# Kernel optimization log

Measured on AMD Instinct MI355X. Metric: run time of the kernel, lower is better.

Reference implementation:

```python
import jax, jax.numpy as jnp
import numpy as np


def setup_inputs() -> dict:
    key = jax.random.key(0)
    k1, k2, k3, k4, k5 = jax.random.split(key, 5)
    C, Cr = 512, 64  # in_channels, in_channels // 8
    B, W, H = 16, 64, 64
    x = jax.random.normal(k1, (B, C, W, H), dtype=jnp.float32)
    # 1x1 conv == pointwise linear over channels; store as [out, in]
    w1 = jax.random.normal(k2, (Cr, C), dtype=jnp.float32) * (1.0 / np.sqrt(C))
    b1 = jax.random.normal(k3, (Cr,), dtype=jnp.float32) * 0.01
    w2 = jax.random.normal(k4, (C, Cr), dtype=jnp.float32) * (1.0 / np.sqrt(Cr))
    b2 = jax.random.normal(k5, (C,), dtype=jnp.float32) * 0.01
    return {"x": x, "w1": w1, "b1": b1, "w2": w2, "b2": b2}


def reference(x, w1, b1, w2, b2):
    B, C, W, H = x.shape
    # conv1x1: channel reduction C -> C//8
    r = jnp.einsum('bchw,oc->bohw', x, w1) + b1[None, :, None, None]
    q = r.reshape(B, -1, W * H)                      # [B, C', N] query/key/value
    # channel-channel attention map [B, C', C'] (bmm(query, key^T))
    att = jnp.einsum('bcn,bdn->bcd', q, q)
    att = jax.nn.softmax(att, axis=-1)
    out = jnp.einsum('bcd,bdn->bcn', att, q)          # [B, C', N]
    out = out.reshape(B, -1, W, H)
    # conv_out: channel expansion C//8 -> C, plus residual
    out = jnp.einsum('bchw,oc->bohw', out, w2) + b2[None, :, None, None]
    return out + x
```

## Files before the change

### kernel.cpp

```cpp
#include <hip/hip_runtime.h>
#include <math.h>

#define NPIX 4096
#define CIN  512
#define CR   64
#define NB   16

typedef __bf16 bf16x8 __attribute__((ext_vector_type(8)));
typedef float  f32x4  __attribute__((ext_vector_type(4)));
typedef float  f32x16 __attribute__((ext_vector_type(16)));
typedef unsigned int uint;
typedef uint   uint4v __attribute__((ext_vector_type(4)));
typedef unsigned short ushort;

static const size_t W1B_OFF = 0;
static const size_t Q_OFF   = W1B_OFF + 65536;
static const size_t QT_OFF  = Q_OFF  + (size_t)NB*CR*NPIX*2;
static const size_t ATT_OFF = QT_OFF + (size_t)NB*NPIX*CR*2;
static const size_t MB_OFF  = ATT_OFF + (size_t)NB*CR*CR*4;


static __device__ inline uint pk_bf16(float a, float b) {
    uint r;
    asm volatile("v_cvt_pk_bf16_f32 %0, %1, %2" : "=v"(r) : "v"(a), "v"(b));
    return r;
}

__global__ __launch_bounds__(256) void k0_cast(const float* __restrict__ w1,
                                               uint* __restrict__ w1b) {
    int i = blockIdx.x * 256 + threadIdx.x;
    w1b[i] = pk_bf16(w1[2 * i], w1[2 * i + 1]);
}

#define K1_LOAD(XV, AF, KS) do {                                             \
    int k0_ = (KS) * 32 + kg * 8;                                            \
    _Pragma("unroll")                                                        \
    for (int pf = 0; pf < 4; pf++) {                                         \
        const float* xp_ = xb + (size_t)k0_ * NPIX + pf * 16;                \
        _Pragma("unroll")                                                    \
        for (int j = 0; j < 8; j++) XV[pf][j] = xp_[(size_t)j * NPIX];       \
    }                                                                        \
    _Pragma("unroll")                                                        \
    for (int of = 0; of < 4; of++)                                           \
        AF[of] = *(const bf16x8*)(w1b + (size_t)(of * 16 + lo) * CIN + k0_); \
} while (0)

#define K1_COMPUTE(XV, AF) do {                                              \
    _Pragma("unroll")                                                        \
    for (int pf = 0; pf < 4; pf++) {                                         \
        uint4v bu_;                                                          \
        _Pragma("unroll")                                                    \
        for (int j = 0; j < 4; j++)                                          \
            bu_[j] = pk_bf16(XV[pf][2 * j], XV[pf][2 * j + 1]);              \
        bf16x8 bf_ = __builtin_bit_cast(bf16x8, bu_);                        \
        _Pragma("unroll")                                                    \
        for (int of = 0; of < 4; of++)                                       \
            acc[pf][of] = __builtin_amdgcn_mfma_f32_16x16x32_bf16(           \
                AF[of], bf_, acc[pf][of], 0, 0, 0);                          \
    }                                                                        \
} while (0)

__global__ __launch_bounds__(256) void k1_conv1(const float* __restrict__ x,
                                                const ushort* __restrict__ w1b,
                                                const float* __restrict__ b1,
                                                ushort* __restrict__ q,
                                                uint2* __restrict__ qt4) {
    int b = blockIdx.y;
    int t = threadIdx.x;
    int wid = t >> 6, l = t & 63;
    int lo = l & 15, kg = l >> 4;
    int px0 = blockIdx.x * 256 + wid * 64;
    const float* xb = x + (size_t)b * CIN * NPIX + px0 + lo;

    f32x4 acc[4][4] = {};
    float xvA[4][8], xvB[4][8];
    bf16x8 afA[4], afB[4];

    K1_LOAD(xvA, afA, 0);
#pragma unroll
    for (int ks2 = 0; ks2 < 8; ks2++) {
        K1_LOAD(xvB, afB, 2 * ks2 + 1);
        K1_COMPUTE(xvA, afA);
        if (ks2 < 7) K1_LOAD(xvA, afA, 2 * ks2 + 2);
        K1_COMPUTE(xvB, afB);
    }

#pragma unroll
    for (int pf = 0; pf < 4; pf++) {
        int px = px0 + pf * 16 + lo;
        ushort* qb = q + (size_t)b * CR * NPIX + px;
        uint2* qt4b = qt4 + (((size_t)b * 256 + (px0 >> 4) + pf) * 4) * 64 + kg * 16 + lo;
#pragma unroll
        for (int of = 0; of < 4; of++) {
            int o = of * 16 + kg * 4;
            float v0 = acc[pf][of][0] + b1[o + 0];
            float v1 = acc[pf][of][1] + b1[o + 1];
            float v2 = acc[pf][of][2] + b1[o + 2];
            float v3 = acc[pf][of][3] + b1[o + 3];
            uint p0 = pk_bf16(v0, v1), p1 = pk_bf16(v2, v3);
            qb[(size_t)(o + 0) * NPIX] = (ushort)(p0 & 0xffff);
            qb[(size_t)(o + 1) * NPIX] = (ushort)(p0 >> 16);
            qb[(size_t)(o + 2) * NPIX] = (ushort)(p1 & 0xffff);
            qb[(size_t)(o + 3) * NPIX] = (ushort)(p1 >> 16);
            qt4b[of * 64] = make_uint2(p0, p1);
        }
    }
}

__global__ __launch_bounds__(1024) void k2_att(const ushort* __restrict__ q,
                                               float* __restrict__ att) {
    __shared__ float part[8][64][66];
    int b = blockIdx.x;
    int t = threadIdx.x;
    int w = t >> 6, l = t & 63;
    int lo = l & 15, kg = l >> 4;
    const ushort* qb = q + (size_t)b * CR * NPIX + w * 256;

    f32x4 acc[4][4] = {};
#pragma unroll 2
    for (int ks = 0; ks < 8; ks++) {
        bf16x8 fr[4];
#pragma unroll
        for (int cf = 0; cf < 4; cf++)
            fr[cf] = *(const bf16x8*)(qb + (size_t)(cf * 16 + lo) * NPIX + ks * 32 + kg * 8);
#pragma unroll
        for (int cf = 0; cf < 4; cf++)
#pragma unroll
            for (int df = 0; df < 4; df++)
                acc[cf][df] = __builtin_amdgcn_mfma_f32_16x16x32_bf16(fr[cf], fr[df], acc[cf][df], 0, 0, 0);
    }
    if (w < 8) {
#pragma unroll
        for (int cf = 0; cf < 4; cf++)
#pragma unroll
            for (int df = 0; df < 4; df++)
#pragma unroll
                for (int r = 0; r < 4; r++)
                    part[w][cf * 16 + kg * 4 + r][df * 16 + lo] = acc[cf][df][r];
    }
    __syncthreads();
    if (w >= 8) {
        int ws = w - 8;
#pragma unroll
        for (int cf = 0; cf < 4; cf++)
#pragma unroll
            for (int df = 0; df < 4; df++)
#pragma unroll
                for (int r = 0; r < 4; r++)
                    part[ws][cf * 16 + kg * 4 + r][df * 16 + lo] += acc[cf][df][r];
    }
    __syncthreads();

#pragma unroll
    for (int i = 0; i < 4; i++) {
        int c = w * 4 + i;
        float v = 0.f;
#pragma unroll
        for (int pw = 0; pw < 8; pw++) v += part[pw][c][l];
        float m = v;
#pragma unroll
        for (int s = 1; s < 64; s <<= 1) m = fmaxf(m, __shfl_xor(m, s, 64));
        float e = __expf(v - m);
        float ssum = e;
#pragma unroll
        for (int s = 1; s < 64; s <<= 1) ssum += __shfl_xor(ssum, s, 64);
        att[((size_t)b * CR + c) * CR + l] = e / ssum;
    }
}

__global__ __launch_bounds__(256) void k3_m(const float* __restrict__ w2,
                                            const float* __restrict__ att,
                                            ushort* __restrict__ mb) {
    int b = blockIdx.y;
    int c  = (blockIdx.x >> 2) * 256 + threadIdx.x;
    int dg = (blockIdx.x & 3) * 16;
    const float* ab  = att + (size_t)b * CR * CR + dg;
    const float* w2r = w2 + (size_t)c * CR;
    float acc[16];
#pragma unroll
    for (int j = 0; j < 16; j++) acc[j] = 0.f;
    for (int k = 0; k < CR; k++) {
        float wv = w2r[k];
#pragma unroll
        for (int j4 = 0; j4 < 4; j4++) {
            f32x4 av = *(const f32x4*)(ab + k * CR + j4 * 4);
#pragma unroll
            for (int u = 0; u < 4; u++)
                acc[j4 * 4 + u] = fmaf(wv, av[u], acc[j4 * 4 + u]);
        }
    }
    uint* mp = (uint*)(mb + ((size_t)b * CIN + c) * CR + dg);
#pragma unroll
    for (int i = 0; i < 8; i++)
        mp[i] = pk_bf16(acc[2 * i], acc[2 * i + 1]);
}

#define K4_LOAD(AF, XR, CC8) do {                                            \
    int c0_ = (cch * 8 + (CC8)) * 32;                                        \
    const ushort* mrow_ = mb + ((size_t)b * CIN + c0_ + l31) * CR;           \
    _Pragma("unroll")                                                        \
    for (int ks = 0; ks < 4; ks++)                                           \
        AF[ks] = *(const bf16x8*)(mrow_ + ks * 16 + lhi * 8);                \
    _Pragma("unroll")                                                        \
    for (int r = 0; r < 16; r++) {                                           \
        int rowD_ = (r & 3) + 8 * (r >> 2) + 4 * lhi;                        \
        XR[r] = x[((size_t)b * CIN + c0_ + rowD_) * NPIX + px];              \
    }                                                                        \
} while (0)

#define K4_STORE(AF, XR, CC8) do {                                           \
    int c0_ = (cch * 8 + (CC8)) * 32;                                        \
    f32x16 acc_ = {};                                                        \
    _Pragma("unroll")                                                        \
    for (int ks = 0; ks < 4; ks++)                                           \
        acc_ = __builtin_amdgcn_mfma_f32_32x32x16_bf16(AF[ks], bf[ks], acc_, 0, 0, 0); \
    _Pragma("unroll")                                                        \
    for (int r = 0; r < 16; r++) {                                           \
        int rowD_ = (r & 3) + 8 * (r >> 2) + 4 * lhi;                        \
        int c_ = c0_ + rowD_;                                                \
        size_t off_ = ((size_t)b * CIN + c_) * NPIX + px;                    \
        y[off_] = acc_[r] + b2[c_] + XR[r];                                  \
    }                                                                        \
} while (0)

__global__ __launch_bounds__(256) void k4_out(const uint2* __restrict__ qt4,
                                              const ushort* __restrict__ mb,
                                              const float* __restrict__ b2,
                                              const float* __restrict__ x,
                                              float* __restrict__ y) {
    int cch = blockIdx.x;
    int b = blockIdx.z;
    int t = threadIdx.x;
    int wid = t >> 6, l = t & 63;
    int l31 = l & 31, lhi = l >> 5;
    int pxblk = blockIdx.y * 128 + wid * 32;
    int px = pxblk + l31;
    const uint2* qt4b = qt4 + (size_t)b * 65536;
    int pxhi = (pxblk >> 4) + ((l >> 4) & 1);
    int pxlo = l & 15;
    int kg2 = lhi * 2;

    bf16x8 bf[4];
#pragma unroll
    for (int ks = 0; ks < 4; ks++) {
        const uint2* p_ = qt4b + (((size_t)pxhi * 4 + ks) * 4 + kg2) * 16 + pxlo;
        uint2 g0 = p_[0], g1 = p_[16];
        uint4v u; u[0] = g0.x; u[1] = g0.y; u[2] = g1.x; u[3] = g1.y;
        bf[ks] = __builtin_bit_cast(bf16x8, u);
    }

    bf16x8 afA[4], afB[4];
    float xrA[16], xrB[16];
    K4_LOAD(afA, xrA, 0);
#pragma unroll
    for (int i2 = 0; i2 < 4; i2++) {
        K4_LOAD(afB, xrB, 2 * i2 + 1);
        K4_STORE(afA, xrA, 2 * i2);
        if (i2 < 3) K4_LOAD(afA, xrA, 2 * i2 + 2);
        K4_STORE(afB, xrB, 2 * i2 + 1);
    }
}

extern "C" void kernel_launch(void* const* d_in, const int* in_sizes, int n_in,
                              void* d_out, int out_size, void* d_ws, size_t ws_size,
                              hipStream_t stream) {
    const float* x  = (const float*)d_in[0];
    const float* w1 = (const float*)d_in[1];
    const float* b1 = (const float*)d_in[2];
    const float* w2 = (const float*)d_in[3];
    const float* b2 = (const float*)d_in[4];
    float* y = (float*)d_out;
    char* ws = (char*)d_ws;

    uint*   w1b = (uint*)  (ws + W1B_OFF);
    ushort* q   = (ushort*)(ws + Q_OFF);
    uint2*  qt4 = (uint2*) (ws + QT_OFF);
    float*  att = (float*) (ws + ATT_OFF);
    ushort* mb  = (ushort*)(ws + MB_OFF);

    hipLaunchKernelGGL(k0_cast,  dim3(64),         dim3(256),  0, stream, w1, w1b);
    hipLaunchKernelGGL(k1_conv1, dim3(16, 16),     dim3(256),  0, stream, x, (const ushort*)w1b, b1, q, qt4);
    hipLaunchKernelGGL(k2_att,   dim3(16),         dim3(1024), 0, stream, q, att);
    hipLaunchKernelGGL(k3_m,     dim3(8, 16),      dim3(256),  0, stream, w2, att, mb);
    hipLaunchKernelGGL(k4_out,   dim3(2, 32, 16),  dim3(256),  0, stream, qt4, mb, b2, x, y);
}
```

Measured before the change: 113.8 us.

## Fuse w1 bf16 cast into conv1 and give each k4 block all output channels

Drops the separate w1 cast kernel: conv1 now loads fp32 w1 directly and converts it to bf16 in registers before each MFMA. The output kernel no longer splits the channel dimension across two blocks, so each block loops over all 16 channel chunks and reads its q tile only once. This removes one launch and halves the k4 grid, but adds redundant weight conversion in every conv1 block and lowers parallelism in k4.

```diff
diff --git a/kernel.cpp b/kernel.cpp
--- a/kernel.cpp
+++ b/kernel.cpp
@@ -13,8 +13,7 @@
 typedef uint   uint4v __attribute__((ext_vector_type(4)));
 typedef unsigned short ushort;
 
-static const size_t W1B_OFF = 0;
-static const size_t Q_OFF   = W1B_OFF + 65536;
+static const size_t Q_OFF   = 65536;
 static const size_t QT_OFF  = Q_OFF  + (size_t)NB*CR*NPIX*2;
 static const size_t ATT_OFF = QT_OFF + (size_t)NB*NPIX*CR*2;
 static const size_t MB_OFF  = ATT_OFF + (size_t)NB*CR*CR*4;
@@ -26,13 +25,7 @@
     return r;
 }
 
-__global__ __launch_bounds__(256) void k0_cast(const float* __restrict__ w1,
-                                               uint* __restrict__ w1b) {
-    int i = blockIdx.x * 256 + threadIdx.x;
-    w1b[i] = pk_bf16(w1[2 * i], w1[2 * i + 1]);
-}
-
-#define K1_LOAD(XV, AF, KS) do {                                             \
+#define K1_LOAD(XV, WF, KS) do {                                             \
     int k0_ = (KS) * 32 + kg * 8;                                            \
     _Pragma("unroll")                                                        \
     for (int pf = 0; pf < 4; pf++) {                                         \
@@ -41,11 +34,24 @@
         for (int j = 0; j < 8; j++) XV[pf][j] = xp_[(size_t)j * NPIX];       \
     }                                                                        \
     _Pragma("unroll")                                                        \
-    for (int of = 0; of < 4; of++)                                           \
-        AF[of] = *(const bf16x8*)(w1b + (size_t)(of * 16 + lo) * CIN + k0_); \
-} while (0)
-
-#define K1_COMPUTE(XV, AF) do {                                              \
+    for (int of = 0; of < 4; of++) {                                         \
+        const float* wp_ = w1 + (size_t)(of * 16 + lo) * CIN + k0_;          \
+        WF[of][0] = *(const f32x4*)wp_;                                      \
+        WF[of][1] = *(const f32x4*)(wp_ + 4);                                \
+    }                                                                        \
+} while (0)
+
+#define K1_COMPUTE(XV, WF) do {                                              \
+    bf16x8 af_[4];                                                           \
+    _Pragma("unroll")                                                        \
+    for (int of = 0; of < 4; of++) {                                         \
+        uint4v au_;                                                          \
+        au_[0] = pk_bf16(WF[of][0][0], WF[of][0][1]);                        \
+        au_[1] = pk_bf16(WF[of][0][2], WF[of][0][3]);                        \
+        au_[2] = pk_bf16(WF[of][1][0], WF[of][1][1]);                        \
+        au_[3] = pk_bf16(WF[of][1][2], WF[of][1][3]);                        \
+        af_[of] = __builtin_bit_cast(bf16x8, au_);                           \
+    }                                                                        \
     _Pragma("unroll")                                                        \
     for (int pf = 0; pf < 4; pf++) {                                         \
         uint4v bu_;                                                          \
@@ -56,12 +62,12 @@
         _Pragma("unroll")                                                    \
         for (int of = 0; of < 4; of++)                                       \
             acc[pf][of] = __builtin_amdgcn_mfma_f32_16x16x32_bf16(           \
-                AF[of], bf_, acc[pf][of], 0, 0, 0);                          \
+                af_[of], bf_, acc[pf][of], 0, 0, 0);                         \
     }                                                                        \
 } while (0)
 
 __global__ __launch_bounds__(256) void k1_conv1(const float* __restrict__ x,
-                                                const ushort* __restrict__ w1b,
+                                                const float* __restrict__ w1,
                                                 const float* __restrict__ b1,
                                                 ushort* __restrict__ q,
                                                 uint2* __restrict__ qt4) {
@@ -74,15 +80,15 @@
 
     f32x4 acc[4][4] = {};
     float xvA[4][8], xvB[4][8];
-    bf16x8 afA[4], afB[4];
-
-    K1_LOAD(xvA, afA, 0);
+    f32x4 wfA[4][2], wfB[4][2];
+
+    K1_LOAD(xvA, wfA, 0);
 #pragma unroll
     for (int ks2 = 0; ks2 < 8; ks2++) {
-        K1_LOAD(xvB, afB, 2 * ks2 + 1);
-        K1_COMPUTE(xvA, afA);
-        if (ks2 < 7) K1_LOAD(xvA, afA, 2 * ks2 + 2);
-        K1_COMPUTE(xvB, afB);
+        K1_LOAD(xvB, wfB, 2 * ks2 + 1);
+        K1_COMPUTE(xvA, wfA);
+        if (ks2 < 7) K1_LOAD(xvA, wfA, 2 * ks2 + 2);
+        K1_COMPUTE(xvB, wfB);
     }
 
 #pragma unroll
@@ -195,8 +201,8 @@
         mp[i] = pk_bf16(acc[2 * i], acc[2 * i + 1]);
 }
 
-#define K4_LOAD(AF, XR, CC8) do {                                            \
-    int c0_ = (cch * 8 + (CC8)) * 32;                                        \
+#define K4_LOAD(AF, XR, CC) do {                                             \
+    int c0_ = (CC) * 32;                                                     \
     const ushort* mrow_ = mb + ((size_t)b * CIN + c0_ + l31) * CR;           \
     _Pragma("unroll")                                                        \
     for (int ks = 0; ks < 4; ks++)                                           \
@@ -208,8 +214,8 @@
     }                                                                        \
 } while (0)
 
-#define K4_STORE(AF, XR, CC8) do {                                           \
-    int c0_ = (cch * 8 + (CC8)) * 32;                                        \
+#define K4_STORE(AF, XR, CC) do {                                            \
+    int c0_ = (CC) * 32;                                                     \
     f32x16 acc_ = {};                                                        \
     _Pragma("unroll")                                                        \
     for (int ks = 0; ks < 4; ks++)                                           \
@@ -228,12 +234,11 @@
                                               const float* __restrict__ b2,
                                               const float* __restrict__ x,
                                               float* __restrict__ y) {
-    int cch = blockIdx.x;
-    int b = blockIdx.z;
+    int b = blockIdx.y;
     int t = threadIdx.x;
     int wid = t >> 6, l = t & 63;
     int l31 = l & 31, lhi = l >> 5;
-    int pxblk = blockIdx.y * 128 + wid * 32;
+    int pxblk = blockIdx.x * 128 + wid * 32;
     int px = pxblk + l31;
     const uint2* qt4b = qt4 + (size_t)b * 65536;
     int pxhi = (pxblk >> 4) + ((l >> 4) & 1);
@@ -253,10 +258,10 @@
     float xrA[16], xrB[16];
     K4_LOAD(afA, xrA, 0);
 #pragma unroll
-    for (int i2 = 0; i2 < 4; i2++) {
+    for (int i2 = 0; i2 < 8; i2++) {
         K4_LOAD(afB, xrB, 2 * i2 + 1);
         K4_STORE(afA, xrA, 2 * i2);
-        if (i2 < 3) K4_LOAD(afA, xrA, 2 * i2 + 2);
+        if (i2 < 7) K4_LOAD(afA, xrA, 2 * i2 + 2);
         K4_STORE(afB, xrB, 2 * i2 + 1);
     }
 }
@@ -272,15 +277,13 @@
     float* y = (float*)d_out;
     char* ws = (char*)d_ws;
 
-    uint*   w1b = (uint*)  (ws + W1B_OFF);
     ushort* q   = (ushort*)(ws + Q_OFF);
     uint2*  qt4 = (uint2*) (ws + QT_OFF);
     float*  att = (float*) (ws + ATT_OFF);
     ushort* mb  = (ushort*)(ws + MB_OFF);
 
-    hipLaunchKernelGGL(k0_cast,  dim3(64),         dim3(256),  0, stream, w1, w1b);
-    hipLaunchKernelGGL(k1_conv1, dim3(16, 16),     dim3(256),  0, stream, x, (const ushort*)w1b, b1, q, qt4);
-    hipLaunchKernelGGL(k2_att,   dim3(16),         dim3(1024), 0, stream, q, att);
-    hipLaunchKernelGGL(k3_m,     dim3(8, 16),      dim3(256),  0, stream, w2, att, mb);
-    hipLaunchKernelGGL(k4_out,   dim3(2, 32, 16),  dim3(256),  0, stream, qt4, mb, b2, x, y);
-}
+    hipLaunchKernelGGL(k1_conv1, dim3(16, 16),  dim3(256),  0, stream, x, w1, b1, q, qt4);
+    hipLaunchKernelGGL(k2_att,   dim3(16),      dim3(1024), 0, stream, q, att);
+    hipLaunchKernelGGL(k3_m,     dim3(8, 16),   dim3(256),  0, stream, w2, att, mb);
+    hipLaunchKernelGGL(k4_out,   dim3(32, 16),  dim3(256),  0, stream, qt4, mb, b2, x, y);
+}
```

Result: no change. 112.9 us (-0.8%).
